# Performance work log

Measured on AMD Instinct MI355X. Metric: run time of the kernel, lower is better.

## Reference

```python
import jax, jax.numpy as jnp
import numpy as np

N = 100_000      # nodes
E = 3_200_000    # edges (avg degree 32)
F_IN = 64        # num_node_features
G = 256          # graphs in batch


def _lin(key, fan_in, fan_out):
    kw, kb = jax.random.split(key)
    bound = 1.0 / np.sqrt(fan_in)
    W = jax.random.uniform(kw, (fan_in, fan_out), jnp.float32, -bound, bound)
    b = jax.random.uniform(kb, (fan_out,), jnp.float32, -bound, bound)
    return W, b


def setup_inputs() -> dict:
    key = jax.random.key(0)
    ks = jax.random.split(key, 9)
    x = jax.random.normal(ks[0], (N, F_IN), jnp.float32)
    edge_index = jax.random.randint(ks[1], (2, E), 0, N, dtype=jnp.int64)
    batch = jnp.sort(jax.random.randint(ks[2], (N,), 0, G, dtype=jnp.int64))
    W1, b1 = _lin(ks[3], F_IN, 60)
    W2, b2 = _lin(ks[4], 60, 50)
    Wf1, bf1 = _lin(ks[5], 50, 30)
    Wf2, bf2 = _lin(ks[6], 30, 20)
    Wf3, bf3 = _lin(ks[7], 20, 10)
    Wo, bo = _lin(ks[8], 10, 1)
    return {"x": x, "edge_index": edge_index, "batch": batch,
            "W1": W1, "b1": b1, "W2": W2, "b2": b2,
            "Wf1": Wf1, "bf1": bf1, "Wf2": Wf2, "bf2": bf2,
            "Wf3": Wf3, "bf3": bf3, "Wo": Wo, "bo": bo}


def _gcn_norm(edge_index, n_nodes):
    # add self loops, then symmetric D^{-1/2} (A+I) D^{-1/2} edge weights
    loop = jnp.arange(n_nodes, dtype=edge_index.dtype)
    src = jnp.concatenate([edge_index[0], loop])
    dst = jnp.concatenate([edge_index[1], loop])
    deg = jax.ops.segment_sum(jnp.ones_like(dst, dtype=jnp.float32), dst,
                              num_segments=n_nodes)
    dinv = jax.lax.rsqrt(deg)  # deg >= 1 thanks to self loops
    norm = dinv[src] * dinv[dst]
    return src, dst, norm


def _gcn_conv(h, W, b, src, dst, norm, n_nodes):
    h = h @ W                                            # [N, out]
    msg = h[src] * norm[:, None]                         # gather over edges
    agg = jax.ops.segment_sum(msg, dst, num_segments=n_nodes)
    return agg + b


def reference(x, edge_index, batch, W1, b1, W2, b2,
              Wf1, bf1, Wf2, bf2, Wf3, bf3, Wo, bo):
    n_nodes = x.shape[0]
    src, dst, norm = _gcn_norm(edge_index, n_nodes)
    h = _gcn_conv(x, W1, b1, src, dst, norm, n_nodes)    # [N, 60]
    h = _gcn_conv(h, W2, b2, src, dst, norm, n_nodes)    # [N, 50]
    # global_add_pool over graph ids
    g = jax.ops.segment_sum(h, batch, num_segments=G)    # [G, 50]
    # MLP stack (no nonlinearities in the original forward)
    g = g @ Wf1 + bf1
    g = g @ Wf2 + bf2
    g = g @ Wf3 + bf3
    return g @ Wo + bo                                   # [G, 1]
```

## Files before the change

### kernel.cpp

```cpp
#include <hip/hip_runtime.h>


#define RSHIFT 7
#define RNODES 128
#define NB_MAX 1024
#define STHREADS 512
#define CTHREADS 512
#define STAGE_CAP 8192
#define BCAP 6144

__global__ void collapse_weights_k(
    const float* __restrict__ W1, const float* __restrict__ b1,
    const float* __restrict__ W2, const float* __restrict__ b2,
    const float* __restrict__ Wf1, const float* __restrict__ bf1,
    const float* __restrict__ Wf2, const float* __restrict__ bf2,
    const float* __restrict__ Wf3, const float* __restrict__ bf3,
    const float* __restrict__ Wo, const float* __restrict__ bo,
    float* __restrict__ w1c, float* __restrict__ sc,
    int* __restrict__ cursor, float* __restrict__ out, int G)
{
    __shared__ float wo[10], w3[20], w2[30], w1[50], w2c[60];
    __shared__ float c0s;
    const int t = threadIdx.x;
    for (int b = t; b < NB_MAX; b += 64) cursor[b] = 0;
    if (t < 10) wo[t] = Wo[t];
    __syncthreads();
    if (t < 20) { float s = 0.f; for (int j = 0; j < 10; ++j) s += Wf3[t*10+j]*wo[j]; w3[t] = s; }
    __syncthreads();
    if (t < 30) { float s = 0.f; for (int j = 0; j < 20; ++j) s += Wf2[t*20+j]*w3[j]; w2[t] = s; }
    __syncthreads();
    if (t < 50) { float s = 0.f; for (int j = 0; j < 30; ++j) s += Wf1[t*30+j]*w2[j]; w1[t] = s; }
    __syncthreads();
    if (t < 60) { float s = 0.f; for (int j = 0; j < 50; ++j) s += W2[t*50+j]*w1[j]; w2c[t] = s; }
    __syncthreads();
    { float s = 0.f; for (int j = 0; j < 60; ++j) s += W1[t*60+j]*w2c[j]; w1c[t] = s; }
    if (t == 0) {
        float c1 = 0.f; for (int j = 0; j < 60; ++j) c1 += b1[j]*w2c[j];
        float c2 = 0.f; for (int j = 0; j < 50; ++j) c2 += b2[j]*w1[j];
        float c0 = bo[0];
        for (int j = 0; j < 30; ++j) c0 += bf1[j]*w2[j];
        for (int j = 0; j < 20; ++j) c0 += bf2[j]*w3[j];
        for (int j = 0; j < 10; ++j) c0 += bf3[j]*wo[j];
        sc[0] = c1; sc[1] = c2; sc[2] = c0;
        c0s = c0;
    }
    __syncthreads();
    for (int g = t; g < G; g += 64) out[g] = c0s;
}

#define LOAD_QUAD(ii, cc, P0, P1, P2, P3, B0, B1, B2, B3, R0, R1, R2, R3)     \
    if (cc == 4) {                                                            \
        int4 s4 = *reinterpret_cast<const int4*>(src + ii);                   \
        int4 d4 = *reinterpret_cast<const int4*>(dst + ii);                   \
        P0 = (unsigned)s4.x | ((unsigned)(d4.x & (RNODES-1)) << 17);          \
        P1 = (unsigned)s4.y | ((unsigned)(d4.y & (RNODES-1)) << 17);          \
        P2 = (unsigned)s4.z | ((unsigned)(d4.z & (RNODES-1)) << 17);          \
        P3 = (unsigned)s4.w | ((unsigned)(d4.w & (RNODES-1)) << 17);          \
        B0 = d4.x >> RSHIFT; B1 = d4.y >> RSHIFT;                             \
        B2 = d4.z >> RSHIFT; B3 = d4.w >> RSHIFT;                             \
        R0 = atomicAdd(&hist[B0], 1);                                         \
        R1 = atomicAdd(&hist[B1], 1);                                         \
        R2 = atomicAdd(&hist[B2], 1);                                         \
        R3 = atomicAdd(&hist[B3], 1);                                         \
    } else {                                                                  \
        if (cc > 0) { int s=src[ii],   d=dst[ii];   P0=(unsigned)s|((unsigned)(d&(RNODES-1))<<17); B0=d>>RSHIFT; R0=atomicAdd(&hist[B0],1); } \
        if (cc > 1) { int s=src[ii+1], d=dst[ii+1]; P1=(unsigned)s|((unsigned)(d&(RNODES-1))<<17); B1=d>>RSHIFT; R1=atomicAdd(&hist[B1],1); } \
        if (cc > 2) { int s=src[ii+2], d=dst[ii+2]; P2=(unsigned)s|((unsigned)(d&(RNODES-1))<<17); B2=d>>RSHIFT; R2=atomicAdd(&hist[B2],1); } \
    }

#define STORE_QUAD(cc, P0, P1, P2, P3, B0, B1, B2, B3, R0, R1, R2, R3)        \
    if (cc > 0) { int s2 = tbase[B0] + R0; staged[s2] = P0; bof[s2] = (unsigned short)B0; } \
    if (cc > 1) { int s2 = tbase[B1] + R1; staged[s2] = P1; bof[s2] = (unsigned short)B1; } \
    if (cc > 2) { int s2 = tbase[B2] + R2; staged[s2] = P2; bof[s2] = (unsigned short)B2; } \
    if (cc > 3) { int s2 = tbase[B3] + R3; staged[s2] = P3; bof[s2] = (unsigned short)B3; }

__global__ __launch_bounds__(STHREADS, 4)
void scatter_u_k(const float* __restrict__ x, const float* __restrict__ w1c,
                 float* __restrict__ u,
                 const int* __restrict__ src, const int* __restrict__ dst,
                 int E, int n, int npb, int nb,
                 int* __restrict__ cursor, unsigned int* __restrict__ binned) {
    __shared__ int hist[NB_MAX];
    __shared__ int tbase[NB_MAX];
    __shared__ int adj[NB_MAX];
    __shared__ int sums[STHREADS];
    __shared__ unsigned int staged[STAGE_CAP];
    __shared__ unsigned short bof[STAGE_CAP];
    const int tid = threadIdx.x;
    const int bx = blockIdx.x;

    {
        const int grp = tid >> 4, sub = tid & 15;
        float4 wv = *reinterpret_cast<const float4*>(w1c + sub * 4);
        int base = bx * npb;
        for (int p = 0; p * 32 < npb; ++p) {
            int nl = p * 32 + grp;
            int g = base + nl;
            bool ok = (nl < npb) && (g < n);
            float val = 0.f;
            if (ok) {
                float4 xv = *reinterpret_cast<const float4*>(
                    x + (size_t)g * 64 + sub * 4);
                val = xv.x*wv.x + xv.y*wv.y + xv.z*wv.z + xv.w*wv.w;
            }
            val += __shfl_down(val, 8, 16);
            val += __shfl_down(val, 4, 16);
            val += __shfl_down(val, 2, 16);
            val += __shfl_down(val, 1, 16);
            if (ok && sub == 0) u[g] = val;
        }
    }

    hist[tid] = 0; hist[tid + STHREADS] = 0;
    __syncthreads();
    int e0 = bx * STAGE_CAP;
    int e1 = e0 + STAGE_CAP; if (e1 > E) e1 = E;

    unsigned pa0=0,pa1=0,pa2=0,pa3=0, pb0=0,pb1=0,pb2=0,pb3=0;
    unsigned pc0=0,pc1=0,pc2=0,pc3=0, pd0=0,pd1=0,pd2=0,pd3=0;
    int ba0=0,ba1=0,ba2=0,ba3=0, bb0=0,bb1=0,bb2=0,bb3=0;
    int bc0=0,bc1=0,bc2=0,bc3=0, bd0=0,bd1=0,bd2=0,bd3=0;
    int ra0=0,ra1=0,ra2=0,ra3=0, rb0=0,rb1=0,rb2=0,rb3=0;
    int rc0=0,rc1=0,rc2=0,rc3=0, rd0=0,rd1=0,rd2=0,rd3=0;

    int iA = e0 + tid * 4;
    int iB = iA + STHREADS * 4;
    int iC = iB + STHREADS * 4;
    int iD = iC + STHREADS * 4;
    int cA = e1 - iA; if (cA > 4) cA = 4; if (cA < 0) cA = 0;
    int cB = e1 - iB; if (cB > 4) cB = 4; if (cB < 0) cB = 0;
    int cC = e1 - iC; if (cC > 4) cC = 4; if (cC < 0) cC = 0;
    int cD = e1 - iD; if (cD > 4) cD = 4; if (cD < 0) cD = 0;

    LOAD_QUAD(iA, cA, pa0,pa1,pa2,pa3, ba0,ba1,ba2,ba3, ra0,ra1,ra2,ra3)
    LOAD_QUAD(iB, cB, pb0,pb1,pb2,pb3, bb0,bb1,bb2,bb3, rb0,rb1,rb2,rb3)
    LOAD_QUAD(iC, cC, pc0,pc1,pc2,pc3, bc0,bc1,bc2,bc3, rc0,rc1,rc2,rc3)
    LOAD_QUAD(iD, cD, pd0,pd1,pd2,pd3, bd0,bd1,bd2,bd3, rd0,rd1,rd2,rd3)
    __syncthreads();

    int h0 = hist[2*tid], h1 = hist[2*tid+1];
    int pair = h0 + h1;
    sums[tid] = pair;
    __syncthreads();
    for (int off = 1; off < STHREADS; off <<= 1) {
        int a = (tid >= off) ? sums[tid - off] : 0;
        __syncthreads();
        sums[tid] += a;
        __syncthreads();
    }
    int excl = sums[tid] - pair;
    tbase[2*tid] = excl;
    tbase[2*tid+1] = excl + h0;
    {
        int b0 = 2*tid, b1 = 2*tid + 1;
        if (b0 < nb && h0 > 0) {
            int r = atomicAdd(&cursor[b0], h0);
            adj[b0] = b0 * BCAP + r - excl;
        }
        if (b1 < nb && h1 > 0) {
            int r = atomicAdd(&cursor[b1], h1);
            adj[b1] = b1 * BCAP + r - (excl + h0);
        }
    }
    __syncthreads();

    STORE_QUAD(cA, pa0,pa1,pa2,pa3, ba0,ba1,ba2,ba3, ra0,ra1,ra2,ra3)
    STORE_QUAD(cB, pb0,pb1,pb2,pb3, bb0,bb1,bb2,bb3, rb0,rb1,rb2,rb3)
    STORE_QUAD(cC, pc0,pc1,pc2,pc3, bc0,bc1,bc2,bc3, rc0,rc1,rc2,rc3)
    STORE_QUAD(cD, pd0,pd1,pd2,pd3, bd0,bd1,bd2,bd3, rd0,rd1,rd2,rd3)
    __syncthreads();

    int tcount = e1 - e0;
    for (int s2 = tid; s2 < tcount; s2 += STHREADS) {
        int b = bof[s2];
        binned[adj[b] + s2] = staged[s2];
    }
}

__global__ __launch_bounds__(CTHREADS, 8)
void degree_dinv_k(const unsigned int* __restrict__ binned,
                   const int* __restrict__ cursor,
                   const float* __restrict__ u,
                   float* __restrict__ dinv, float* __restrict__ w, int n) {
    __shared__ int cnt[RNODES];
    int tid = threadIdx.x, b = blockIdx.x;
    if (tid < RNODES) cnt[tid] = 0;
    __syncthreads();
    size_t s0 = (size_t)b * BCAP;
    int c = cursor[b];
    if (c > BCAP) c = BCAP;
    int nvec = c >> 2;
    uint4 pA, pB, pC;
    bool aA = tid < nvec, aB = tid + CTHREADS < nvec, aC = tid + 2*CTHREADS < nvec;
    if (aA) pA = *reinterpret_cast<const uint4*>(binned + s0 + 4 * (size_t)tid);
    if (aB) pB = *reinterpret_cast<const uint4*>(binned + s0 + 4 * (size_t)(tid + CTHREADS));
    if (aC) pC = *reinterpret_cast<const uint4*>(binned + s0 + 4 * (size_t)(tid + 2*CTHREADS));
    if (aA) {
        atomicAdd(&cnt[pA.x >> 17], 1); atomicAdd(&cnt[pA.y >> 17], 1);
        atomicAdd(&cnt[pA.z >> 17], 1); atomicAdd(&cnt[pA.w >> 17], 1);
    }
    if (aB) {
        atomicAdd(&cnt[pB.x >> 17], 1); atomicAdd(&cnt[pB.y >> 17], 1);
        atomicAdd(&cnt[pB.z >> 17], 1); atomicAdd(&cnt[pB.w >> 17], 1);
    }
    if (aC) {
        atomicAdd(&cnt[pC.x >> 17], 1); atomicAdd(&cnt[pC.y >> 17], 1);
        atomicAdd(&cnt[pC.z >> 17], 1); atomicAdd(&cnt[pC.w >> 17], 1);
    }
    int i = 4 * nvec + tid;
    if (i < c) atomicAdd(&cnt[binned[s0 + i] >> 17], 1);
    __syncthreads();
    int g = (b << RSHIFT) + tid;
    if (tid < RNODES && g < n) {
        float d = rsqrtf((float)(cnt[tid] + 1));
        dinv[g] = d;
        w[g] = d * u[g];
    }
}

__global__ __launch_bounds__(CTHREADS, 8)
void conv_mid_k(const unsigned int* __restrict__ binned,
                const int* __restrict__ cursor,
                const float* __restrict__ w, const float* __restrict__ dinv,
                const float* __restrict__ u, const float* __restrict__ sc,
                float* __restrict__ v, float* __restrict__ wb, int n) {
    __shared__ float acc[RNODES];
    int tid = threadIdx.x, b = blockIdx.x;
    if (tid < RNODES) acc[tid] = 0.f;
    __syncthreads();
    size_t s0 = (size_t)b * BCAP;
    int cnt = cursor[b];
    if (cnt > BCAP) cnt = BCAP;
    int nvec = cnt >> 2;
    uint4 pA, pB, pC;
    bool aA = tid < nvec, aB = tid + CTHREADS < nvec, aC = tid + 2*CTHREADS < nvec;
    if (aA) pA = *reinterpret_cast<const uint4*>(binned + s0 + 4 * (size_t)tid);
    if (aB) pB = *reinterpret_cast<const uint4*>(binned + s0 + 4 * (size_t)(tid + CTHREADS));
    if (aC) pC = *reinterpret_cast<const uint4*>(binned + s0 + 4 * (size_t)(tid + 2*CTHREADS));
    float wa0=0,wa1=0,wa2=0,wa3=0, wb0=0,wb1=0,wb2=0,wb3=0, wc0=0,wc1=0,wc2=0,wc3=0;
    if (aA) { wa0=w[pA.x & 0x1FFFF]; wa1=w[pA.y & 0x1FFFF]; wa2=w[pA.z & 0x1FFFF]; wa3=w[pA.w & 0x1FFFF]; }
    if (aB) { wb0=w[pB.x & 0x1FFFF]; wb1=w[pB.y & 0x1FFFF]; wb2=w[pB.z & 0x1FFFF]; wb3=w[pB.w & 0x1FFFF]; }
    if (aC) { wc0=w[pC.x & 0x1FFFF]; wc1=w[pC.y & 0x1FFFF]; wc2=w[pC.z & 0x1FFFF]; wc3=w[pC.w & 0x1FFFF]; }
    if (aA) {
        atomicAdd(&acc[pA.x >> 17], wa0); atomicAdd(&acc[pA.y >> 17], wa1);
        atomicAdd(&acc[pA.z >> 17], wa2); atomicAdd(&acc[pA.w >> 17], wa3);
    }
    if (aB) {
        atomicAdd(&acc[pB.x >> 17], wb0); atomicAdd(&acc[pB.y >> 17], wb1);
        atomicAdd(&acc[pB.z >> 17], wb2); atomicAdd(&acc[pB.w >> 17], wb3);
    }
    if (aC) {
        atomicAdd(&acc[pC.x >> 17], wc0); atomicAdd(&acc[pC.y >> 17], wc1);
        atomicAdd(&acc[pC.z >> 17], wc2); atomicAdd(&acc[pC.w >> 17], wc3);
    }
    int i = 4 * nvec + tid;
    if (i < cnt) { unsigned p = binned[s0 + i]; atomicAdd(&acc[p >> 17], w[p & 0x1FFFF]); }
    __syncthreads();
    int g = (b << RSHIFT) + tid;
    if (tid < RNODES && g < n) {
        float di = dinv[g];
        float val = sc[0] + di * acc[tid] + di * di * u[g];
        v[g] = val;
        wb[g] = di * val;
    }
}

__global__ __launch_bounds__(CTHREADS, 8)
void conv_final_k(const unsigned int* __restrict__ binned,
                  const int* __restrict__ cursor,
                  const float* __restrict__ wbv, const float* __restrict__ dinv,
                  const float* __restrict__ v, const float* __restrict__ sc,
                  const int* __restrict__ batch, float* __restrict__ out, int n) {
    __shared__ float acc[RNODES];
    __shared__ float tbuf[RNODES];
    __shared__ int gbuf[RNODES];
    int tid = threadIdx.x, b = blockIdx.x;
    if (tid < RNODES) acc[tid] = 0.f;
    __syncthreads();
    size_t s0 = (size_t)b * BCAP;
    int cnt = cursor[b];
    if (cnt > BCAP) cnt = BCAP;
    int nvec = cnt >> 2;
    uint4 pA, pB, pC;
    bool aA = tid < nvec, aB = tid + CTHREADS < nvec, aC = tid + 2*CTHREADS < nvec;
    if (aA) pA = *reinterpret_cast<const uint4*>(binned + s0 + 4 * (size_t)tid);
    if (aB) pB = *reinterpret_cast<const uint4*>(binned + s0 + 4 * (size_t)(tid + CTHREADS));
    if (aC) pC = *reinterpret_cast<const uint4*>(binned + s0 + 4 * (size_t)(tid + 2*CTHREADS));
    float wa0=0,wa1=0,wa2=0,wa3=0, wb0=0,wb1=0,wb2=0,wb3=0, wc0=0,wc1=0,wc2=0,wc3=0;
    if (aA) { wa0=wbv[pA.x & 0x1FFFF]; wa1=wbv[pA.y & 0x1FFFF]; wa2=wbv[pA.z & 0x1FFFF]; wa3=wbv[pA.w & 0x1FFFF]; }
    if (aB) { wb0=wbv[pB.x & 0x1FFFF]; wb1=wbv[pB.y & 0x1FFFF]; wb2=wbv[pB.z & 0x1FFFF]; wb3=wbv[pB.w & 0x1FFFF]; }
    if (aC) { wc0=wbv[pC.x & 0x1FFFF]; wc1=wbv[pC.y & 0x1FFFF]; wc2=wbv[pC.z & 0x1FFFF]; wc3=wbv[pC.w & 0x1FFFF]; }
    if (aA) {
        atomicAdd(&acc[pA.x >> 17], wa0); atomicAdd(&acc[pA.y >> 17], wa1);
        atomicAdd(&acc[pA.z >> 17], wa2); atomicAdd(&acc[pA.w >> 17], wa3);
    }
    if (aB) {
        atomicAdd(&acc[pB.x >> 17], wb0); atomicAdd(&acc[pB.y >> 17], wb1);
        atomicAdd(&acc[pB.z >> 17], wb2); atomicAdd(&acc[pB.w >> 17], wb3);
    }
    if (aC) {
        atomicAdd(&acc[pC.x >> 17], wc0); atomicAdd(&acc[pC.y >> 17], wc1);
        atomicAdd(&acc[pC.z >> 17], wc2); atomicAdd(&acc[pC.w >> 17], wc3);
    }
    int i = 4 * nvec + tid;
    if (i < cnt) { unsigned p = binned[s0 + i]; atomicAdd(&acc[p >> 17], wbv[p & 0x1FFFF]); }
    __syncthreads();
    int g = (b << RSHIFT) + tid;
    float tval = 0.f; int gid = -1;
    if (tid < RNODES && g < n) {
        float di = dinv[g];
        tval = sc[1] + di * acc[tid] + di * di * v[g];
        gid = batch[g];
    }
    if (tid < RNODES) { tbuf[tid] = tval; gbuf[tid] = gid; }
    __syncthreads();
    if (tid < RNODES && g < n) {
        bool head = (tid == 0) || (gbuf[tid - 1] != gid);
        if (head) {
            float s = 0.f;
            int i2 = tid;
            while (i2 < RNODES && gbuf[i2] == gid) { s += tbuf[i2]; ++i2; }
            atomicAdd(&out[gid], s);
        }
    }
}

extern "C" void kernel_launch(void* const* d_in, const int* in_sizes, int n_in,
                              void* d_out, int out_size, void* d_ws, size_t ws_size,
                              hipStream_t stream)
{
    const float* x    = (const float*)d_in[0];
    const int*   ei   = (const int*)d_in[1];
    const int*   batch= (const int*)d_in[2];
    const float* W1   = (const float*)d_in[3];
    const float* b1   = (const float*)d_in[4];
    const float* W2   = (const float*)d_in[5];
    const float* b2   = (const float*)d_in[6];
    const float* Wf1  = (const float*)d_in[7];
    const float* bf1  = (const float*)d_in[8];
    const float* Wf2  = (const float*)d_in[9];
    const float* bf2  = (const float*)d_in[10];
    const float* Wf3  = (const float*)d_in[11];
    const float* bf3  = (const float*)d_in[12];
    const float* Wo   = (const float*)d_in[13];
    const float* bo   = (const float*)d_in[14];
    float* out = (float*)d_out;

    const int n = in_sizes[0] / 64;
    const int E = in_sizes[1] / 2;
    const int G = out_size;
    const int* src = ei;
    const int* dst = ei + E;
    const int nb = (n + RNODES - 1) >> RSHIFT;

    float* ws_f = (float*)d_ws;
    int*   ws_i = (int*)d_ws;
    float* w1c    = ws_f;
    float* sc     = ws_f + 64;
    int*   cursor = ws_i + 128;
    size_t off_u  = 128 + (size_t)NB_MAX;
    float* u      = ws_f + off_u;
    float* dinv   = u + n;
    float* w      = dinv + n;
    float* v      = w + n;
    float* wb     = v + n;
    size_t off_b  = off_u + 5*(size_t)n;
    off_b = (off_b + 3) & ~(size_t)3;
    unsigned int* binned = (unsigned int*)(ws_f + off_b);

    const int NT = (E + STAGE_CAP - 1) / STAGE_CAP;
    const int npb = (n + NT - 1) / NT;

    hipLaunchKernelGGL(collapse_weights_k, dim3(1), dim3(64), 0, stream,
                       W1, b1, W2, b2, Wf1, bf1, Wf2, bf2, Wf3, bf3, Wo, bo,
                       w1c, sc, cursor, out, G);
    hipLaunchKernelGGL(scatter_u_k, dim3(NT), dim3(STHREADS), 0, stream,
                       x, w1c, u, src, dst, E, n, npb, nb, cursor, binned);
    hipLaunchKernelGGL(degree_dinv_k, dim3(nb), dim3(CTHREADS), 0, stream,
                       binned, cursor, u, dinv, w, n);
    hipLaunchKernelGGL(conv_mid_k, dim3(nb), dim3(CTHREADS), 0, stream,
                       binned, cursor, w, dinv, u, sc, v, wb, n);
    hipLaunchKernelGGL(conv_final_k, dim3(nb), dim3(CTHREADS), 0, stream,
                       binned, cursor, wb, dinv, v, sc, batch, out, n);
}
```

Measured before the change: 207.0 us.

## Counting-sort binned edges per destination to replace LDS atomics with segmented sums

The degree kernel now does a full in-block counting sort of each bin's packed edges by destination node. It writes the sorted edges back to global memory along with per-node offsets. Both convolution passes then reduce each node's neighbours with four lanes and shuffles, instead of issuing LDS float atomics per edge. This trades an extra read and write pass over the binned edges, plus 48KB of LDS per block in the sort kernel, for atomic-free aggregation in the two conv kernels.

```diff
diff --git a/kernel.cpp b/kernel.cpp
--- a/kernel.cpp
+++ b/kernel.cpp
@@ -177,89 +177,108 @@
     }
 }
 
-__global__ __launch_bounds__(CTHREADS, 8)
-void degree_dinv_k(const unsigned int* __restrict__ binned,
-                   const int* __restrict__ cursor,
-                   const float* __restrict__ u,
-                   float* __restrict__ dinv, float* __restrict__ w, int n) {
+__global__ __launch_bounds__(CTHREADS, 4)
+void sort_dinv_k(unsigned int* __restrict__ binned,
+                 const int* __restrict__ cursor,
+                 const float* __restrict__ u,
+                 float* __restrict__ dinv, float* __restrict__ w,
+                 int* __restrict__ offG, int n) {
+    __shared__ unsigned eIn[BCAP];
+    __shared__ unsigned eOut[BCAP];
     __shared__ int cnt[RNODES];
-    int tid = threadIdx.x, b = blockIdx.x;
+    __shared__ int off[RNODES];
+    __shared__ int pos[RNODES];
+    const int tid = threadIdx.x, b = blockIdx.x;
     if (tid < RNODES) cnt[tid] = 0;
     __syncthreads();
     size_t s0 = (size_t)b * BCAP;
     int c = cursor[b];
     if (c > BCAP) c = BCAP;
     int nvec = c >> 2;
-    uint4 pA, pB, pC;
-    bool aA = tid < nvec, aB = tid + CTHREADS < nvec, aC = tid + 2*CTHREADS < nvec;
-    if (aA) pA = *reinterpret_cast<const uint4*>(binned + s0 + 4 * (size_t)tid);
-    if (aB) pB = *reinterpret_cast<const uint4*>(binned + s0 + 4 * (size_t)(tid + CTHREADS));
-    if (aC) pC = *reinterpret_cast<const uint4*>(binned + s0 + 4 * (size_t)(tid + 2*CTHREADS));
-    if (aA) {
-        atomicAdd(&cnt[pA.x >> 17], 1); atomicAdd(&cnt[pA.y >> 17], 1);
-        atomicAdd(&cnt[pA.z >> 17], 1); atomicAdd(&cnt[pA.w >> 17], 1);
-    }
-    if (aB) {
-        atomicAdd(&cnt[pB.x >> 17], 1); atomicAdd(&cnt[pB.y >> 17], 1);
-        atomicAdd(&cnt[pB.z >> 17], 1); atomicAdd(&cnt[pB.w >> 17], 1);
-    }
-    if (aC) {
-        atomicAdd(&cnt[pC.x >> 17], 1); atomicAdd(&cnt[pC.y >> 17], 1);
-        atomicAdd(&cnt[pC.z >> 17], 1); atomicAdd(&cnt[pC.w >> 17], 1);
-    }
-    int i = 4 * nvec + tid;
-    if (i < c) atomicAdd(&cnt[binned[s0 + i] >> 17], 1);
-    __syncthreads();
-    int g = (b << RSHIFT) + tid;
-    if (tid < RNODES && g < n) {
-        float d = rsqrtf((float)(cnt[tid] + 1));
-        dinv[g] = d;
-        w[g] = d * u[g];
+    for (int k = tid; k < nvec; k += CTHREADS) {
+        uint4 p = *reinterpret_cast<const uint4*>(binned + s0 + 4 * (size_t)k);
+        eIn[4*k+0] = p.x; eIn[4*k+1] = p.y; eIn[4*k+2] = p.z; eIn[4*k+3] = p.w;
+        atomicAdd(&cnt[p.x >> 17], 1);
+        atomicAdd(&cnt[p.y >> 17], 1);
+        atomicAdd(&cnt[p.z >> 17], 1);
+        atomicAdd(&cnt[p.w >> 17], 1);
+    }
+    for (int i = 4 * nvec + tid; i < c; i += CTHREADS) {
+        unsigned p = binned[s0 + i];
+        eIn[i] = p;
+        atomicAdd(&cnt[p >> 17], 1);
+    }
+    __syncthreads();
+    int hval = (tid < RNODES) ? cnt[tid] : 0;
+    if (tid < RNODES) off[tid] = hval;
+    __syncthreads();
+    for (int o = 1; o < RNODES; o <<= 1) {
+        int a = 0;
+        if (tid < RNODES && tid >= o) a = off[tid - o];
+        __syncthreads();
+        if (tid < RNODES) off[tid] += a;
+        __syncthreads();
+    }
+    if (tid < RNODES) {
+        int e = off[tid] - hval;
+        off[tid] = e;
+        pos[tid] = e;
+    }
+    __syncthreads();
+    for (int i = tid; i < c; i += CTHREADS) {
+        unsigned p = eIn[i];
+        int r = atomicAdd(&pos[p >> 17], 1);
+        eOut[r] = p;
+    }
+    __syncthreads();
+    for (int k = tid; k < nvec; k += CTHREADS) {
+        uint4 p;
+        p.x = eOut[4*k+0]; p.y = eOut[4*k+1]; p.z = eOut[4*k+2]; p.w = eOut[4*k+3];
+        *reinterpret_cast<uint4*>(binned + s0 + 4 * (size_t)k) = p;
+    }
+    for (int i = 4 * nvec + tid; i < c; i += CTHREADS)
+        binned[s0 + i] = eOut[i];
+    if (tid < RNODES) {
+        int g = (b << RSHIFT) + tid;
+        if (g < n) {
+            float d = rsqrtf((float)(cnt[tid] + 1));
+            dinv[g] = d;
+            w[g] = d * u[g];
+            offG[g] = off[tid];
+        }
     }
 }
 
 __global__ __launch_bounds__(CTHREADS, 8)
 void conv_mid_k(const unsigned int* __restrict__ binned,
-                const int* __restrict__ cursor,
+                const int* __restrict__ cursor, const int* __restrict__ offG,
                 const float* __restrict__ w, const float* __restrict__ dinv,
                 const float* __restrict__ u, const float* __restrict__ sc,
                 float* __restrict__ v, float* __restrict__ wb, int n) {
-    __shared__ float acc[RNODES];
+    __shared__ int off_s[RNODES + 1];
     int tid = threadIdx.x, b = blockIdx.x;
-    if (tid < RNODES) acc[tid] = 0.f;
-    __syncthreads();
     size_t s0 = (size_t)b * BCAP;
-    int cnt = cursor[b];
-    if (cnt > BCAP) cnt = BCAP;
-    int nvec = cnt >> 2;
-    uint4 pA, pB, pC;
-    bool aA = tid < nvec, aB = tid + CTHREADS < nvec, aC = tid + 2*CTHREADS < nvec;
-    if (aA) pA = *reinterpret_cast<const uint4*>(binned + s0 + 4 * (size_t)tid);
-    if (aB) pB = *reinterpret_cast<const uint4*>(binned + s0 + 4 * (size_t)(tid + CTHREADS));
-    if (aC) pC = *reinterpret_cast<const uint4*>(binned + s0 + 4 * (size_t)(tid + 2*CTHREADS));
-    float wa0=0,wa1=0,wa2=0,wa3=0, wb0=0,wb1=0,wb2=0,wb3=0, wc0=0,wc1=0,wc2=0,wc3=0;
-    if (aA) { wa0=w[pA.x & 0x1FFFF]; wa1=w[pA.y & 0x1FFFF]; wa2=w[pA.z & 0x1FFFF]; wa3=w[pA.w & 0x1FFFF]; }
-    if (aB) { wb0=w[pB.x & 0x1FFFF]; wb1=w[pB.y & 0x1FFFF]; wb2=w[pB.z & 0x1FFFF]; wb3=w[pB.w & 0x1FFFF]; }
-    if (aC) { wc0=w[pC.x & 0x1FFFF]; wc1=w[pC.y & 0x1FFFF]; wc2=w[pC.z & 0x1FFFF]; wc3=w[pC.w & 0x1FFFF]; }
-    if (aA) {
-        atomicAdd(&acc[pA.x >> 17], wa0); atomicAdd(&acc[pA.y >> 17], wa1);
-        atomicAdd(&acc[pA.z >> 17], wa2); atomicAdd(&acc[pA.w >> 17], wa3);
-    }
-    if (aB) {
-        atomicAdd(&acc[pB.x >> 17], wb0); atomicAdd(&acc[pB.y >> 17], wb1);
-        atomicAdd(&acc[pB.z >> 17], wb2); atomicAdd(&acc[pB.w >> 17], wb3);
-    }
-    if (aC) {
-        atomicAdd(&acc[pC.x >> 17], wc0); atomicAdd(&acc[pC.y >> 17], wc1);
-        atomicAdd(&acc[pC.z >> 17], wc2); atomicAdd(&acc[pC.w >> 17], wc3);
-    }
-    int i = 4 * nvec + tid;
-    if (i < cnt) { unsigned p = binned[s0 + i]; atomicAdd(&acc[p >> 17], w[p & 0x1FFFF]); }
-    __syncthreads();
-    int g = (b << RSHIFT) + tid;
-    if (tid < RNODES && g < n) {
+    int c = cursor[b];
+    if (c > BCAP) c = BCAP;
+    if (tid < RNODES) {
+        int g = (b << RSHIFT) + tid;
+        off_s[tid] = (g < n) ? offG[g] : c;
+    }
+    if (tid == 0) off_s[RNODES] = c;
+    __syncthreads();
+    int node = tid >> 2, sub = tid & 3;
+    int g = (b << RSHIFT) + node;
+    int o0 = off_s[node], o1 = off_s[node + 1];
+    float s = 0.f;
+    for (int k = o0 + sub; k < o1; k += 4) {
+        unsigned p = binned[s0 + k];
+        s += w[p & 0x1FFFF];
+    }
+    s += __shfl_xor(s, 1, 4);
+    s += __shfl_xor(s, 2, 4);
+    if (sub == 0 && g < n) {
         float di = dinv[g];
-        float val = sc[0] + di * acc[tid] + di * di * u[g];
+        float val = sc[0] + di * s + di * di * u[g];
         v[g] = val;
         wb[g] = di * val;
     }
@@ -267,60 +286,55 @@
 
 __global__ __launch_bounds__(CTHREADS, 8)
 void conv_final_k(const unsigned int* __restrict__ binned,
-                  const int* __restrict__ cursor,
+                  const int* __restrict__ cursor, const int* __restrict__ offG,
                   const float* __restrict__ wbv, const float* __restrict__ dinv,
                   const float* __restrict__ v, const float* __restrict__ sc,
                   const int* __restrict__ batch, float* __restrict__ out, int n) {
-    __shared__ float acc[RNODES];
+    __shared__ int off_s[RNODES + 1];
     __shared__ float tbuf[RNODES];
     __shared__ int gbuf[RNODES];
     int tid = threadIdx.x, b = blockIdx.x;
-    if (tid < RNODES) acc[tid] = 0.f;
-    __syncthreads();
     size_t s0 = (size_t)b * BCAP;
-    int cnt = cursor[b];
-    if (cnt > BCAP) cnt = BCAP;
-    int nvec = cnt >> 2;
-    uint4 pA, pB, pC;
-    bool aA = tid < nvec, aB = tid + CTHREADS < nvec, aC = tid + 2*CTHREADS < nvec;
-    if (aA) pA = *reinterpret_cast<const uint4*>(binned + s0 + 4 * (size_t)tid);
-    if (aB) pB = *reinterpret_cast<const uint4*>(binned + s0 + 4 * (size_t)(tid + CTHREADS));
-    if (aC) pC = *reinterpret_cast<const uint4*>(binned + s0 + 4 * (size_t)(tid + 2*CTHREADS));
-    float wa0=0,wa1=0,wa2=0,wa3=0, wb0=0,wb1=0,wb2=0,wb3=0, wc0=0,wc1=0,wc2=0,wc3=0;
-    if (aA) { wa0=wbv[pA.x & 0x1FFFF]; wa1=wbv[pA.y & 0x1FFFF]; wa2=wbv[pA.z & 0x1FFFF]; wa3=wbv[pA.w & 0x1FFFF]; }
-    if (aB) { wb0=wbv[pB.x & 0x1FFFF]; wb1=wbv[pB.y & 0x1FFFF]; wb2=wbv[pB.z & 0x1FFFF]; wb3=wbv[pB.w & 0x1FFFF]; }
-    if (aC) { wc0=wbv[pC.x & 0x1FFFF]; wc1=wbv[pC.y & 0x1FFFF]; wc2=wbv[pC.z & 0x1FFFF]; wc3=wbv[pC.w & 0x1FFFF]; }
-    if (aA) {
-        atomicAdd(&acc[pA.x >> 17], wa0); atomicAdd(&acc[pA.y >> 17], wa1);
-        atomicAdd(&acc[pA.z >> 17], wa2); atomicAdd(&acc[pA.w >> 17], wa3);
-    }
-    if (aB) {
-        atomicAdd(&acc[pB.x >> 17], wb0); atomicAdd(&acc[pB.y >> 17], wb1);
-        atomicAdd(&acc[pB.z >> 17], wb2); atomicAdd(&acc[pB.w >> 17], wb3);
-    }
-    if (aC) {
-        atomicAdd(&acc[pC.x >> 17], wc0); atomicAdd(&acc[pC.y >> 17], wc1);
-        atomicAdd(&acc[pC.z >> 17], wc2); atomicAdd(&acc[pC.w >> 17], wc3);
-    }
-    int i = 4 * nvec + tid;
-    if (i < cnt) { unsigned p = binned[s0 + i]; atomicAdd(&acc[p >> 17], wbv[p & 0x1FFFF]); }
-    __syncthreads();
-    int g = (b << RSHIFT) + tid;
-    float tval = 0.f; int gid = -1;
-    if (tid < RNODES && g < n) {
-        float di = dinv[g];
-        tval = sc[1] + di * acc[tid] + di * di * v[g];
-        gid = batch[g];
-    }
-    if (tid < RNODES) { tbuf[tid] = tval; gbuf[tid] = gid; }
-    __syncthreads();
-    if (tid < RNODES && g < n) {
-        bool head = (tid == 0) || (gbuf[tid - 1] != gid);
-        if (head) {
-            float s = 0.f;
-            int i2 = tid;
-            while (i2 < RNODES && gbuf[i2] == gid) { s += tbuf[i2]; ++i2; }
-            atomicAdd(&out[gid], s);
+    int c = cursor[b];
+    if (c > BCAP) c = BCAP;
+    if (tid < RNODES) {
+        int g = (b << RSHIFT) + tid;
+        off_s[tid] = (g < n) ? offG[g] : c;
+    }
+    if (tid == 0) off_s[RNODES] = c;
+    __syncthreads();
+    int node = tid >> 2, sub = tid & 3;
+    int g = (b << RSHIFT) + node;
+    int o0 = off_s[node], o1 = off_s[node + 1];
+    float s = 0.f;
+    for (int k = o0 + sub; k < o1; k += 4) {
+        unsigned p = binned[s0 + k];
+        s += wbv[p & 0x1FFFF];
+    }
+    s += __shfl_xor(s, 1, 4);
+    s += __shfl_xor(s, 2, 4);
+    if (sub == 0) {
+        float tval = 0.f; int gid = -1;
+        if (g < n) {
+            float di = dinv[g];
+            tval = sc[1] + di * s + di * di * v[g];
+            gid = batch[g];
+        }
+        tbuf[node] = tval;
+        gbuf[node] = gid;
+    }
+    __syncthreads();
+    if (tid < RNODES) {
+        int g2 = (b << RSHIFT) + tid;
+        if (g2 < n) {
+            int gid = gbuf[tid];
+            bool head = (tid == 0) || (gbuf[tid - 1] != gid);
+            if (head) {
+                float sum = 0.f;
+                int i2 = tid;
+                while (i2 < RNODES && gbuf[i2] == gid) { sum += tbuf[i2]; ++i2; }
+                atomicAdd(&out[gid], sum);
+            }
         }
     }
 }
@@ -364,7 +378,8 @@
     float* w      = dinv + n;
     float* v      = w + n;
     float* wb     = v + n;
-    size_t off_b  = off_u + 5*(size_t)n;
+    int*   offG   = ws_i + off_u + 5*(size_t)n;
+    size_t off_b  = off_u + 6*(size_t)n;
     off_b = (off_b + 3) & ~(size_t)3;
     unsigned int* binned = (unsigned int*)(ws_f + off_b);
 
@@ -376,10 +391,10 @@
                        w1c, sc, cursor, out, G);
     hipLaunchKernelGGL(scatter_u_k, dim3(NT), dim3(STHREADS), 0, stream,
                        x, w1c, u, src, dst, E, n, npb, nb, cursor, binned);
-    hipLaunchKernelGGL(degree_dinv_k, dim3(nb), dim3(CTHREADS), 0, stream,
-                       binned, cursor, u, dinv, w, n);
+    hipLaunchKernelGGL(sort_dinv_k, dim3(nb), dim3(CTHREADS), 0, stream,
+                       binned, cursor, u, dinv, w, offG, n);
     hipLaunchKernelGGL(conv_mid_k, dim3(nb), dim3(CTHREADS), 0, stream,
-                       binned, cursor, w, dinv, u, sc, v, wb, n);
+                       binned, cursor, offG, w, dinv, u, sc, v, wb, n);
     hipLaunchKernelGGL(conv_final_k, dim3(nb), dim3(CTHREADS), 0, stream,
-                       binned, cursor, wb, dinv, v, sc, batch, out, n);
-}
+                       binned, cursor, offG, wb, dinv, v, sc, batch, out, n);
+}
```

New measurement: 206.5 us. Within noise of the previous version (-0.2%).
